# Kernel tuning notes

Measured on AMD Instinct MI355X. Metric: run time of the kernel, lower is better.

## Reference

```python
import jax, jax.numpy as jnp
import numpy as np

PRED_LEN = 6

def conv2d_same(x, w):
    # x: (B,H,W,Cin), w: (kh,kw,Cin,Cout) -> (B,H,W,Cout)
    return jax.lax.conv_general_dilated(
        x, w, window_strides=(1, 1), padding='SAME',
        dimension_numbers=('NHWC', 'HWIO', 'NHWC'))

def setup_inputs() -> dict:
    key = jax.random.key(0)
    ks = jax.random.split(key, 6)
    B, T, H, W, C = 8, 12, 128, 128, 1
    F = 64
    s_in = 1.0 / np.sqrt(3 * 3 * C)
    s_rec = 1.0 / np.sqrt(3 * 3 * F)
    return {
        'x': jax.random.normal(ks[0], (B, T, H, W, C), jnp.float32),
        'kernel': jax.random.normal(ks[1], (3, 3, C, 4 * F), jnp.float32) * s_in,
        'rec_kernel': jax.random.normal(ks[2], (3, 3, F, 4 * F), jnp.float32) * s_rec,
        'bias': jnp.zeros((4 * F,), jnp.float32),
        'w_out': jax.random.normal(ks[3], (3, 3, F, 1), jnp.float32) * s_rec,
        'b_out': jnp.zeros((1,), jnp.float32),
        'w_proj': jax.random.normal(ks[4], (1, 1, 1, F), jnp.float32),
        'b_proj': jnp.zeros((F,), jnp.float32),
    }

def reference(x, kernel, rec_kernel, bias, w_out, b_out, w_proj, b_proj):
    B, T, H, W, C = x.shape
    F = rec_kernel.shape[2]

    def step(carry, xt):
        h, c = carry
        # fused gate pre-activations: (B,H,W,4F), Keras gate order i,f,g,o
        z = conv2d_same(xt, kernel) + conv2d_same(h, rec_kernel) + bias
        i, f, g, o = jnp.split(z, 4, axis=-1)
        c_new = jax.nn.sigmoid(f) * c + jax.nn.sigmoid(i) * jnp.tanh(g)
        h_new = jax.nn.sigmoid(o) * jnp.tanh(c_new)
        return (h_new, c_new), None

    h0 = jnp.zeros((B, H, W, F), x.dtype)
    c0 = jnp.zeros((B, H, W, F), x.dtype)
    (h, c), _ = jax.lax.scan(step, (h0, c0), jnp.moveaxis(x, 1, 0))

    preds = []
    cur = h
    for _ in range(PRED_LEN):
        pred = jax.nn.sigmoid(conv2d_same(cur, w_out) + b_out)  # (B,H,W,1)
        preds.append(pred)
        cur = jax.nn.relu(conv2d_same(pred, w_proj) + b_proj)   # (B,H,W,F)
    return jnp.stack(preds, axis=1)  # (B,PRED_LEN,H,W,1)
```

## Files before the change

### kernel.cpp

```cpp
#include <hip/hip_runtime.h>
#include <math.h>

#define BB 8
#define TT 12
#define HH 128
#define WW 128
#define FF 64
#define GG 256
#define PRED_LEN 6
#define TW 64

typedef __attribute__((ext_vector_type(8))) short short8;
typedef __attribute__((ext_vector_type(4))) float floatx4;

__device__ __forceinline__ float sigf(float x) { return 1.f / (1.f + __expf(-x)); }
__device__ __forceinline__ float tanhfast(float x) { return 1.f - 2.f / (__expf(2.f * x) + 1.f); }

__device__ __forceinline__ unsigned short f2bf(float x) {
    unsigned u = __float_as_uint(x);
    u = (u + 0x7FFFu + ((u >> 16) & 1u)) >> 16;
    return (unsigned short)u;
}

__global__ __launch_bounds__(256) void pack_wr(
    const float* __restrict__ wr, const float* __restrict__ wk,
    const float* __restrict__ bias, short8* __restrict__ packed)
{
    int e = blockIdx.x * 256 + threadIdx.x;
    if (e >= 19 * 16 * 64) return;
    int lane = e & 63;
    int rest = e >> 6;
    int nt = rest & 15;
    int ch = rest >> 4;
    int col = lane & 15, kpart = lane >> 4;
    int n = nt * 16 + col;
    short8 v;
    if (ch < 18) {
        int kc = ch & 1, tap = ch >> 1;
        #pragma unroll
        for (int j = 0; j < 8; ++j) {
            int k = kc * 32 + kpart * 8 + j;
            v[j] = (short)f2bf(wr[((size_t)(tap * 64 + k)) * GG + n]);
        }
    } else {
        #pragma unroll
        for (int j = 0; j < 8; ++j) {
            int k = kpart * 8 + j;
            unsigned short r = 0;
            if (k < 9) r = f2bf(wk[k * GG + n]);
            else if (k == 9) r = f2bf(bias[n]);
            v[j] = (short)r;
        }
    }
    packed[e] = v;
}

template<bool FIRST>
__global__ __launch_bounds__(256, 4) void lstm_step_mfma(
    const float* __restrict__ x,
    int t,
    const unsigned short* __restrict__ h_in,
    float* __restrict__ c_buf,
    unsigned short* __restrict__ h_out,
    const short8* __restrict__ packedB)
{
    __shared__ __align__(16) unsigned short sh[3 * 66 * FF];
    __shared__ __align__(16) unsigned short sxa[64 * 32];
    __shared__ float sx[3][66];

    const int tid = threadIdx.x;
    const int x0 = blockIdx.x * TW;
    const int y  = blockIdx.y;
    const int b  = blockIdx.z;
    char* shb = (char*)sh;

    if (!FIRST) {
        for (int i = tid; i < 3 * 66 * 8; i += 256) {
            int cq  = i & 7;
            int rc  = i >> 3;
            int col = rc % 66, r = rc / 66;
            int gy = y + r - 1, gx = x0 + col - 1;
            uint4 v = make_uint4(0u, 0u, 0u, 0u);
            if ((unsigned)gy < HH && (unsigned)gx < WW)
                v = *(const uint4*)(h_in + ((((size_t)b * HH + gy) * WW + gx) * FF + cq * 8));
            int byte = ((r * 66 + col) * FF + cq * 8) * 2;
            byte ^= ((col & 7) << 4);
            *(uint4*)(shb + byte) = v;
        }
    }
    for (int i = tid; i < 3 * 66; i += 256) {
        int col = i % 66, r = i / 66;
        int gy = y + r - 1, gx = x0 + col - 1;
        float v = 0.f;
        if ((unsigned)gy < HH && (unsigned)gx < WW)
            v = x[(((size_t)b * TT + t) * HH + gy) * WW + gx];
        sx[r][col] = v;
    }
    __syncthreads();

    {
        int px = tid >> 2, kpc = tid & 3;
        short8 v;
        #pragma unroll
        for (int j = 0; j < 8; ++j) {
            int k = kpc * 8 + j;
            unsigned short r = 0;
            if (k < 9) r = f2bf(sx[k / 3][px + (k % 3)]);
            else if (k == 9) r = (unsigned short)0x3F80;
            v[j] = (short)r;
        }
        int byte = (px * 64 + kpc * 16) ^ ((px & 7) << 4);
        *(short8*)((char*)sxa + byte) = v;
    }
    __syncthreads();

    const int l  = tid & 63;
    const int w  = tid >> 6;
    const int lc = l & 15;
    const int kp = l >> 4;
    const int gcol = w * 16 + lc;

    floatx4 acc[4][4];
    #pragma unroll
    for (int m = 0; m < 4; ++m)
        #pragma unroll
        for (int q = 0; q < 4; ++q)
            acc[m][q] = (floatx4){0.f, 0.f, 0.f, 0.f};

    if (!FIRST) {
        #pragma unroll
        for (int c = 0; c < 18; ++c) {
            const int tap_ = c >> 1, kc_ = c & 1, dy_ = tap_ / 3, dx_ = tap_ % 3;
            short8 af[4], bf[4];
            #pragma unroll
            for (int m_ = 0; m_ < 4; ++m_) {
                const int col_ = m_ * 16 + lc + dx_;
                int byte_ = ((dy_ * 66 + col_) * FF + kc_ * 32 + kp * 8) * 2;
                byte_ ^= ((col_ & 7) << 4);
                af[m_] = *(const short8*)(shb + byte_);
            }
            #pragma unroll
            for (int q_ = 0; q_ < 4; ++q_)
                bf[q_] = packedB[(size_t)(c * 16 + (q_ * 4 + w)) * 64 + l];
            #pragma unroll
            for (int m_ = 0; m_ < 4; ++m_)
                #pragma unroll
                for (int q_ = 0; q_ < 4; ++q_)
                    acc[m_][q_] = __builtin_amdgcn_mfma_f32_16x16x32_bf16(
                        af[m_], bf[q_], acc[m_][q_], 0, 0, 0);
        }
    }
    {
        short8 af[4], bf[4];
        #pragma unroll
        for (int m_ = 0; m_ < 4; ++m_) {
            const int px_ = m_ * 16 + lc;
            int byte_ = (px_ * 64 + kp * 16) ^ ((px_ & 7) << 4);
            af[m_] = *(const short8*)((const char*)sxa + byte_);
        }
        #pragma unroll
        for (int q_ = 0; q_ < 4; ++q_)
            bf[q_] = packedB[(size_t)(18 * 16 + (q_ * 4 + w)) * 64 + l];
        #pragma unroll
        for (int m_ = 0; m_ < 4; ++m_)
            #pragma unroll
            for (int q_ = 0; q_ < 4; ++q_)
                acc[m_][q_] = __builtin_amdgcn_mfma_f32_16x16x32_bf16(
                    af[m_], bf[q_], acc[m_][q_], 0, 0, 0);
    }

    #pragma unroll
    for (int m = 0; m < 4; ++m) {
        #pragma unroll
        for (int r = 0; r < 4; ++r) {
            int p = m * 16 + kp * 4 + r;
            size_t idx = (((size_t)b * HH + y) * WW + (x0 + p)) * FF + gcol;
            float cp = FIRST ? 0.f : c_buf[idx];
            float iv = sigf(acc[m][0][r]);
            float fv = sigf(acc[m][1][r]);
            float gv = tanhfast(acc[m][2][r]);
            float ov = sigf(acc[m][3][r]);
            float cn = fv * cp + iv * gv;
            float hn = ov * tanhfast(cn);
            c_buf[idx] = cn;
            h_out[idx] = f2bf(hn);
        }
    }
}

__global__ __launch_bounds__(256) void dec_fused(
    const unsigned short* __restrict__ cur_in, const float* __restrict__ w_out,
    const float* __restrict__ b_out, const float* __restrict__ w_proj,
    const float* __restrict__ b_proj, float* __restrict__ out,
    unsigned short* __restrict__ cur_out, int ti)
{
    int tid = threadIdx.x;
    int j  = tid & 7;
    int pp = tid >> 3;
    int xx = blockIdx.x * 32 + pp;
    int y = blockIdx.y, b = blockIdx.z;

    float s = 0.f;
    for (int dy = 0; dy < 3; ++dy) {
        int gy = y + dy - 1;
        if ((unsigned)gy >= HH) continue;
        #pragma unroll
        for (int dx = 0; dx < 3; ++dx) {
            int gx = xx + dx - 1;
            if ((unsigned)gx >= WW) continue;
            const uint4 cv = *(const uint4*)(cur_in + ((((size_t)b * HH + gy) * WW + gx) * FF + j * 8));
            const float4* wp = (const float4*)&w_out[(dy * 3 + dx) * FF + j * 8];
            float4 w0 = wp[0], w1 = wp[1];
            unsigned cx = cv.x, cy = cv.y, cz = cv.z, cw = cv.w;
            s += __uint_as_float(cx << 16) * w0.x + __uint_as_float(cx & 0xFFFF0000u) * w0.y
               + __uint_as_float(cy << 16) * w0.z + __uint_as_float(cy & 0xFFFF0000u) * w0.w
               + __uint_as_float(cz << 16) * w1.x + __uint_as_float(cz & 0xFFFF0000u) * w1.y
               + __uint_as_float(cw << 16) * w1.z + __uint_as_float(cw & 0xFFFF0000u) * w1.w;
        }
    }
    s += __shfl_xor(s, 1);
    s += __shfl_xor(s, 2);
    s += __shfl_xor(s, 4);
    float pv = sigf(s + b_out[0]);

    size_t pix = (((size_t)b * HH + y) * WW + xx);
    if (j == 0)
        out[((size_t)b * PRED_LEN + ti) * (HH * WW) + (size_t)y * WW + xx] = pv;

    const float4* wp = (const float4*)w_proj;
    const float4* bp = (const float4*)b_proj;
    float4 w0 = wp[j * 2], w1 = wp[j * 2 + 1];
    float4 b0 = bp[j * 2], b1 = bp[j * 2 + 1];
    short8 o;
    o[0] = (short)f2bf(fmaxf(fmaf(pv, w0.x, b0.x), 0.f));
    o[1] = (short)f2bf(fmaxf(fmaf(pv, w0.y, b0.y), 0.f));
    o[2] = (short)f2bf(fmaxf(fmaf(pv, w0.z, b0.z), 0.f));
    o[3] = (short)f2bf(fmaxf(fmaf(pv, w0.w, b0.w), 0.f));
    o[4] = (short)f2bf(fmaxf(fmaf(pv, w1.x, b1.x), 0.f));
    o[5] = (short)f2bf(fmaxf(fmaf(pv, w1.y, b1.y), 0.f));
    o[6] = (short)f2bf(fmaxf(fmaf(pv, w1.z, b1.z), 0.f));
    o[7] = (short)f2bf(fmaxf(fmaf(pv, w1.w, b1.w), 0.f));
    *(short8*)(cur_out + pix * FF + j * 8) = o;
}

extern "C" void kernel_launch(void* const* d_in, const int* in_sizes, int n_in,
                              void* d_out, int out_size, void* d_ws, size_t ws_size,
                              hipStream_t stream)
{
    const float* x      = (const float*)d_in[0];
    const float* wk     = (const float*)d_in[1];
    const float* wr     = (const float*)d_in[2];
    const float* bias   = (const float*)d_in[3];
    const float* w_out  = (const float*)d_in[4];
    const float* b_out  = (const float*)d_in[5];
    const float* w_proj = (const float*)d_in[6];
    const float* b_proj = (const float*)d_in[7];
    float* out = (float*)d_out;

    const size_t SB = (size_t)BB * HH * WW * FF;
    unsigned short* h_a = (unsigned short*)d_ws;
    unsigned short* h_b = h_a + SB;
    float* cb = (float*)((char*)d_ws + 2 * SB * sizeof(unsigned short));
    short8* packed = (short8*)((char*)cb + SB * sizeof(float));

    pack_wr<<<76, 256, 0, stream>>>(wr, wk, bias, packed);

    dim3 gs(WW / TW, HH, BB);
    unsigned short* bufs[2] = {h_a, h_b};
    lstm_step_mfma<true><<<gs, 256, 0, stream>>>(x, 0, bufs[0], cb, bufs[1], packed);
    for (int t = 1; t < TT; ++t) {
        lstm_step_mfma<false><<<gs, 256, 0, stream>>>(x, t, bufs[t & 1], cb,
                                                      bufs[(t + 1) & 1], packed);
    }

    for (int ti = 0; ti < PRED_LEN; ++ti) {
        dec_fused<<<dim3(WW / 32, HH, BB), 256, 0, stream>>>(
            bufs[ti & 1], w_out, b_out, w_proj, b_proj, out, bufs[(ti + 1) & 1], ti);
    }
}
```

Measured before the change: 831.2 us.

## Halve LSTM tile width, raise occupancy, swizzle block order across XCDs

Cuts the per-block pixel tile from 64 to 32, which halves the accumulators and shared memory per block, and raises the launch-bounds occupancy target from 4 to 8 waves. Both kernels now use a 1D grid with an XCD-aware remap of block index to (batch, row, x-tile), so neighbouring rows share L2 on the same chiplet. The previous cell state is loaded before the MFMA loop so its latency overlaps the compute, and the input-conv step is folded into the main tap loop. The cost is a larger halo overhead per pixel (34 vs 66 columns) and more reloads of the B fragments per output.

```diff
diff --git a/kernel.cpp b/kernel.cpp
--- a/kernel.cpp
+++ b/kernel.cpp
@@ -8,7 +8,7 @@
 #define FF 64
 #define GG 256
 #define PRED_LEN 6
-#define TW 64
+#define TW 32
 
 typedef __attribute__((ext_vector_type(8))) short short8;
 typedef __attribute__((ext_vector_type(4))) float floatx4;
@@ -20,6 +20,14 @@
     unsigned u = __float_as_uint(x);
     u = (u + 0x7FFFu + ((u >> 16) & 1u)) >> 16;
     return (unsigned short)u;
+}
+
+__device__ __forceinline__ void decode_wg(int wg, int& b, int& y, int& x0) {
+    int lin = (wg & 7) * 512 + (wg >> 3);
+    b  = lin >> 9;
+    int rem = lin & 511;
+    y  = rem >> 2;
+    x0 = (rem & 3) * TW;
 }
 
 __global__ __launch_bounds__(256) void pack_wr(
@@ -56,7 +64,7 @@
 }
 
 template<bool FIRST>
-__global__ __launch_bounds__(256, 4) void lstm_step_mfma(
+__global__ __launch_bounds__(256, 8) void lstm_step_mfma(
     const float* __restrict__ x,
     int t,
     const unsigned short* __restrict__ h_in,
@@ -64,32 +72,31 @@
     unsigned short* __restrict__ h_out,
     const short8* __restrict__ packedB)
 {
-    __shared__ __align__(16) unsigned short sh[3 * 66 * FF];
-    __shared__ __align__(16) unsigned short sxa[64 * 32];
-    __shared__ float sx[3][66];
+    __shared__ __align__(16) unsigned short sh[3 * 34 * FF];
+    __shared__ __align__(16) unsigned short sxa[TW * 32];
+    __shared__ float sx[3][34];
 
     const int tid = threadIdx.x;
-    const int x0 = blockIdx.x * TW;
-    const int y  = blockIdx.y;
-    const int b  = blockIdx.z;
+    int b, y, x0;
+    decode_wg(blockIdx.x, b, y, x0);
     char* shb = (char*)sh;
 
     if (!FIRST) {
-        for (int i = tid; i < 3 * 66 * 8; i += 256) {
+        for (int i = tid; i < 3 * 34 * 8; i += 256) {
             int cq  = i & 7;
             int rc  = i >> 3;
-            int col = rc % 66, r = rc / 66;
+            int col = rc % 34, r = rc / 34;
             int gy = y + r - 1, gx = x0 + col - 1;
             uint4 v = make_uint4(0u, 0u, 0u, 0u);
             if ((unsigned)gy < HH && (unsigned)gx < WW)
                 v = *(const uint4*)(h_in + ((((size_t)b * HH + gy) * WW + gx) * FF + cq * 8));
-            int byte = ((r * 66 + col) * FF + cq * 8) * 2;
+            int byte = ((r * 34 + col) * FF + cq * 8) * 2;
             byte ^= ((col & 7) << 4);
             *(uint4*)(shb + byte) = v;
         }
     }
-    for (int i = tid; i < 3 * 66; i += 256) {
-        int col = i % 66, r = i / 66;
+    for (int i = tid; i < 3 * 34; i += 256) {
+        int col = i % 34, r = i / 34;
         int gy = y + r - 1, gx = x0 + col - 1;
         float v = 0.f;
         if ((unsigned)gy < HH && (unsigned)gx < WW)
@@ -98,7 +105,7 @@
     }
     __syncthreads();
 
-    {
+    if (tid < TW * 4) {
         int px = tid >> 2, kpc = tid & 3;
         short8 v;
         #pragma unroll
@@ -119,50 +126,49 @@
     const int lc = l & 15;
     const int kp = l >> 4;
     const int gcol = w * 16 + lc;
-
-    floatx4 acc[4][4];
+    const size_t base = (((size_t)b * HH + y) * WW + x0) * FF + gcol;
+
+    float cp[2][4];
+    if (!FIRST) {
+        #pragma unroll
+        for (int m = 0; m < 2; ++m)
+            #pragma unroll
+            for (int r = 0; r < 4; ++r)
+                cp[m][r] = c_buf[base + (size_t)(m * 16 + kp * 4 + r) * FF];
+    }
+
+    floatx4 acc[2][4];
     #pragma unroll
-    for (int m = 0; m < 4; ++m)
+    for (int m = 0; m < 2; ++m)
         #pragma unroll
         for (int q = 0; q < 4; ++q)
             acc[m][q] = (floatx4){0.f, 0.f, 0.f, 0.f};
 
-    if (!FIRST) {
-        #pragma unroll
-        for (int c = 0; c < 18; ++c) {
+    #pragma unroll
+    for (int c = FIRST ? 18 : 0; c < 19; ++c) {
+        short8 af[2], bf[4];
+        if (c < 18) {
             const int tap_ = c >> 1, kc_ = c & 1, dy_ = tap_ / 3, dx_ = tap_ % 3;
-            short8 af[4], bf[4];
-            #pragma unroll
-            for (int m_ = 0; m_ < 4; ++m_) {
+            #pragma unroll
+            for (int m_ = 0; m_ < 2; ++m_) {
                 const int col_ = m_ * 16 + lc + dx_;
-                int byte_ = ((dy_ * 66 + col_) * FF + kc_ * 32 + kp * 8) * 2;
+                int byte_ = ((dy_ * 34 + col_) * FF + kc_ * 32 + kp * 8) * 2;
                 byte_ ^= ((col_ & 7) << 4);
                 af[m_] = *(const short8*)(shb + byte_);
             }
-            #pragma unroll
-            for (int q_ = 0; q_ < 4; ++q_)
-                bf[q_] = packedB[(size_t)(c * 16 + (q_ * 4 + w)) * 64 + l];
-            #pragma unroll
-            for (int m_ = 0; m_ < 4; ++m_)
-                #pragma unroll
-                for (int q_ = 0; q_ < 4; ++q_)
-                    acc[m_][q_] = __builtin_amdgcn_mfma_f32_16x16x32_bf16(
-                        af[m_], bf[q_], acc[m_][q_], 0, 0, 0);
-        }
-    }
-    {
-        short8 af[4], bf[4];
-        #pragma unroll
-        for (int m_ = 0; m_ < 4; ++m_) {
-            const int px_ = m_ * 16 + lc;
-            int byte_ = (px_ * 64 + kp * 16) ^ ((px_ & 7) << 4);
-            af[m_] = *(const short8*)((const char*)sxa + byte_);
+        } else {
+            #pragma unroll
+            for (int m_ = 0; m_ < 2; ++m_) {
+                const int px_ = m_ * 16 + lc;
+                int byte_ = (px_ * 64 + kp * 16) ^ ((px_ & 7) << 4);
+                af[m_] = *(const short8*)((const char*)sxa + byte_);
+            }
         }
         #pragma unroll
         for (int q_ = 0; q_ < 4; ++q_)
-            bf[q_] = packedB[(size_t)(18 * 16 + (q_ * 4 + w)) * 64 + l];
-        #pragma unroll
-        for (int m_ = 0; m_ < 4; ++m_)
+            bf[q_] = packedB[(size_t)(c * 16 + (q_ * 4 + w)) * 64 + l];
+        #pragma unroll
+        for (int m_ = 0; m_ < 2; ++m_)
             #pragma unroll
             for (int q_ = 0; q_ < 4; ++q_)
                 acc[m_][q_] = __builtin_amdgcn_mfma_f32_16x16x32_bf16(
@@ -170,17 +176,17 @@
     }
 
     #pragma unroll
-    for (int m = 0; m < 4; ++m) {
+    for (int m = 0; m < 2; ++m) {
         #pragma unroll
         for (int r = 0; r < 4; ++r) {
             int p = m * 16 + kp * 4 + r;
-            size_t idx = (((size_t)b * HH + y) * WW + (x0 + p)) * FF + gcol;
-            float cp = FIRST ? 0.f : c_buf[idx];
+            size_t idx = base + (size_t)p * FF;
+            float cpv = FIRST ? 0.f : cp[m][r];
             float iv = sigf(acc[m][0][r]);
             float fv = sigf(acc[m][1][r]);
             float gv = tanhfast(acc[m][2][r]);
             float ov = sigf(acc[m][3][r]);
-            float cn = fv * cp + iv * gv;
+            float cn = fv * cpv + iv * gv;
             float hn = ov * tanhfast(cn);
             c_buf[idx] = cn;
             h_out[idx] = f2bf(hn);
@@ -197,8 +203,9 @@
     int tid = threadIdx.x;
     int j  = tid & 7;
     int pp = tid >> 3;
-    int xx = blockIdx.x * 32 + pp;
-    int y = blockIdx.y, b = blockIdx.z;
+    int b, y, x0;
+    decode_wg(blockIdx.x, b, y, x0);
+    int xx = x0 + pp;
 
     float s = 0.f;
     for (int dy = 0; dy < 3; ++dy) {
@@ -265,16 +272,16 @@
 
     pack_wr<<<76, 256, 0, stream>>>(wr, wk, bias, packed);
 
-    dim3 gs(WW / TW, HH, BB);
+    const int NBLK = (WW / TW) * HH * BB;
     unsigned short* bufs[2] = {h_a, h_b};
-    lstm_step_mfma<true><<<gs, 256, 0, stream>>>(x, 0, bufs[0], cb, bufs[1], packed);
+    lstm_step_mfma<true><<<NBLK, 256, 0, stream>>>(x, 0, bufs[0], cb, bufs[1], packed);
     for (int t = 1; t < TT; ++t) {
-        lstm_step_mfma<false><<<gs, 256, 0, stream>>>(x, t, bufs[t & 1], cb,
-                                                      bufs[(t + 1) & 1], packed);
+        lstm_step_mfma<false><<<NBLK, 256, 0, stream>>>(x, t, bufs[t & 1], cb,
+                                                        bufs[(t + 1) & 1], packed);
     }
 
     for (int ti = 0; ti < PRED_LEN; ++ti) {
-        dec_fused<<<dim3(WW / 32, HH, BB), 256, 0, stream>>>(
+        dec_fused<<<NBLK, 256, 0, stream>>>(
             bufs[ti & 1], w_out, b_out, w_proj, b_proj, out, bufs[(ti + 1) & 1], ti);
     }
 }
```

New measurement: 2.004 ms. 2.41x slower.
